# Performance work log

Hardware: AMD Instinct MI355X
Metric: run time of the kernel (lower is better)

Reference implementation:

```python
import jax, jax.numpy as jnp
import numpy as np

B, S, H, NH, DEPTH = 8, 1024, 1024, 16, 24
MLP = int(H * 4.0)
EPS = 1e-6


def _ln(z):
    # flax LayerNorm(use_bias=False, use_scale=False, dtype=bf16): stats in fp32, output bf16
    m = jnp.mean(z, axis=-1, keepdims=True)
    v = jnp.mean(jnp.square(z - m), axis=-1, keepdims=True)
    return ((z - m) * jax.lax.rsqrt(v + EPS)).astype(jnp.bfloat16)


def _modulate(x, shift, scale):
    return x * scale[:, None] + shift[:, None]


def _rms(x):
    return jnp.sqrt(jnp.mean(jnp.square(x)))


def setup_inputs() -> dict:
    key = jax.random.key(0)
    ks = jax.random.split(key, 7)
    init = lambda k, shape, std: (jax.random.normal(k, shape, dtype=jnp.float32) * std)
    return {
        "x": jax.random.normal(ks[0], (B, S, H), dtype=jnp.float32),
        "c": jax.random.normal(ks[1], (B, H), dtype=jnp.float32),
        "w_cond": init(ks[2], (H, 6 * H), 0.02),
        "w_qkv": init(ks[3], (H, 3 * H), 0.02),
        "w_attn_out": init(ks[4], (H, H), 0.02 / np.sqrt(2 * DEPTH)),
        "w_mlp1": init(ks[5], (H, MLP), 0.02),
        "w_mlp2": init(ks[6], (MLP, H), 0.02 / np.sqrt(2 * DEPTH)),
    }


def reference(x, c, w_cond, w_qkv, w_attn_out, w_mlp1, w_mlp2):
    dh = H // NH
    # adaLN conditioning
    cm = jax.nn.silu(c) @ w_cond  # [B, 6H]
    shift_msa, scale_msa, gate_msa, shift_mlp, scale_mlp, gate_mlp = jnp.split(cm, 6, axis=-1)

    # --- attention ---
    x_mod = _modulate(_ln(x), shift_msa, scale_msa)  # fp32 after promote
    kqv = x_mod @ w_qkv
    k, q, v = jnp.split(kqv, 3, axis=-1)
    k = k.reshape(B, S, NH, dh)
    q = q.reshape(B, S, NH, dh) / jnp.sqrt(jnp.float32(dh))
    v = v.reshape(B, S, NH, dh)
    w = jnp.einsum('bqhc,bkhc->bhqk', q, k).astype(jnp.float32)
    w = jax.nn.softmax(w, axis=-1)
    info_max_attn_weight = jnp.mean(jnp.max(w, axis=-1))
    y = jnp.einsum('bhqk,bkhc->bqhc', w, v).reshape(x.shape)
    x_attn = gate_msa[:, None] * (y @ w_attn_out)
    info_attn_norm_ratio = _rms(x_attn) / _rms(x)
    x = x + x_attn

    # --- MLP ---
    x_mod2 = _modulate(_ln(x), shift_mlp, scale_mlp)
    x_mlp = x_mod2 @ w_mlp1
    frac_pos = jnp.mean(x_mlp > 0, axis=(0, 1))
    info_relu_diff = jnp.mean(jnp.abs(frac_pos - 0.5))
    info_relu_zero = jnp.mean(frac_pos == 0)
    info_relu_positive = jnp.mean(frac_pos == 1)
    info_relu_norm = _rms(x_mlp)
    x_mlp = jax.nn.gelu(x_mlp)
    x_mlp = gate_mlp[:, None] * (x_mlp @ w_mlp2)
    info_mlp_norm_ratio = _rms(x_mlp) / _rms(x)
    x = x + x_mlp
    return (x, (info_relu_diff, info_relu_zero, info_relu_positive,
                info_max_attn_weight, info_attn_norm_ratio, info_mlp_norm_ratio,
                info_relu_norm))
```

## Files before the change

### kernel.cpp

```cpp
#include <hip/hip_runtime.h>

typedef unsigned short u16;
typedef __bf16 bf16x8 __attribute__((ext_vector_type(8)));
typedef unsigned short u16x8 __attribute__((ext_vector_type(8)));
typedef float f32x4 __attribute__((ext_vector_type(4)));

union V8 { u16x8 u; bf16x8 b; };

__device__ __forceinline__ u16 f2bf(float f) {
    unsigned u = __float_as_uint(f);
    u += 0x7fffu + ((u >> 16) & 1u);
    return (u16)(u >> 16);
}
__device__ __forceinline__ float bf2f(u16 h) {
    return __uint_as_float(((unsigned)h) << 16);
}

__device__ __forceinline__ void gld16(const void* g, void* l) {
    __builtin_amdgcn_global_load_lds(
        (const __attribute__((address_space(1))) void*)g,
        (__attribute__((address_space(3))) void*)l, 16, 0, 0);
}

__device__ __forceinline__ float block_sum256(float v, float* red) {
#pragma unroll
    for (int mk = 1; mk < 64; mk <<= 1) v += __shfl_xor(v, mk);
    __syncthreads();
    if ((threadIdx.x & 63) == 0) red[threadIdx.x >> 6] = v;
    __syncthreads();
    return red[0] + red[1] + red[2] + red[3];
}

__global__ __launch_bounds__(256)
void cond_kernel(const float* __restrict__ c, const float* __restrict__ w,
                 float* __restrict__ cm) {
    __shared__ float sc[1024];
    const int b = blockIdx.y;
    for (int i = threadIdx.x; i < 1024; i += 256) {
        float v = c[b * 1024 + i];
        sc[i] = v / (1.f + expf(-v));
    }
    __syncthreads();
    const int col = blockIdx.x * 256 + threadIdx.x;
    float acc = 0.f;
    for (int i = 0; i < 1024; ++i) acc += sc[i] * w[(size_t)i * 6144 + col];
    cm[b * 6144 + col] = acc;
}

__global__ __launch_bounds__(256)
void ln_mod_kernel(const float* __restrict__ x, const float* __restrict__ cm,
                   int shift0, int scale0, u16* __restrict__ out) {
    __shared__ float red[8];
    const int row = blockIdx.x, tid = threadIdx.x;
    const int b = row >> 10;
    const float4 v = *(const float4*)(x + (size_t)row * 1024 + tid * 4);
    float s = v.x + v.y + v.z + v.w;
#pragma unroll
    for (int mk = 1; mk < 64; mk <<= 1) s += __shfl_xor(s, mk);
    if ((tid & 63) == 0) red[tid >> 6] = s;
    __syncthreads();
    const float mean = (red[0] + red[1] + red[2] + red[3]) * (1.f / 1024.f);
    const float d0 = v.x - mean, d1 = v.y - mean, d2 = v.z - mean, d3 = v.w - mean;
    float ss = d0 * d0 + d1 * d1 + d2 * d2 + d3 * d3;
#pragma unroll
    for (int mk = 1; mk < 64; mk <<= 1) ss += __shfl_xor(ss, mk);
    if ((tid & 63) == 0) red[4 + (tid >> 6)] = ss;
    __syncthreads();
    const float var = (red[4] + red[5] + red[6] + red[7]) * (1.f / 1024.f);
    const float rs = rsqrtf(var + 1e-6f);
    const float* cmb = cm + b * 6144;
    const int c0 = tid * 4;
    ushort4 ov;
    ov.x = f2bf(bf2f(f2bf(d0 * rs)) * cmb[scale0 + c0 + 0] + cmb[shift0 + c0 + 0]);
    ov.y = f2bf(bf2f(f2bf(d1 * rs)) * cmb[scale0 + c0 + 1] + cmb[shift0 + c0 + 1]);
    ov.z = f2bf(bf2f(f2bf(d2 * rs)) * cmb[scale0 + c0 + 2] + cmb[shift0 + c0 + 2]);
    ov.w = f2bf(bf2f(f2bf(d3 * rs)) * cmb[scale0 + c0 + 3] + cmb[shift0 + c0 + 3]);
    *(ushort4*)(out + (size_t)row * 1024 + c0) = ov;
}

__global__ __launch_bounds__(256)
void transpose_cast(const float* __restrict__ in, u16* __restrict__ out,
                    int R, int C) {
    __shared__ float t[32][33];
    const int tx = threadIdx.x, ty = threadIdx.y;
    const int c0 = blockIdx.x * 32, r0 = blockIdx.y * 32;
#pragma unroll
    for (int i = 0; i < 4; ++i)
        t[ty + i * 8][tx] = in[(size_t)(r0 + ty + i * 8) * C + c0 + tx];
    __syncthreads();
#pragma unroll
    for (int i = 0; i < 4; ++i)
        out[(size_t)(c0 + ty + i * 8) * R + r0 + tx] = f2bf(t[tx][ty + i * 8]);
}

__global__ __launch_bounds__(256)
void vtrans_kernel(const u16* __restrict__ kqv, u16* __restrict__ vT) {
    __shared__ u16 t[32][33];
    const int tx = threadIdx.x, ty = threadIdx.y;
    const int s0 = blockIdx.x * 32, d0 = blockIdx.y * 32;
    const int bh = blockIdx.z, b = bh >> 4, h = bh & 15;
#pragma unroll
    for (int i = 0; i < 4; ++i) {
        int s = s0 + ty + i * 8;
        t[ty + i * 8][tx] = kqv[(size_t)(b * 1024 + s) * 3072 + 2048 + h * 64 + d0 + tx];
    }
    __syncthreads();
#pragma unroll
    for (int i = 0; i < 4; ++i) {
        int d = d0 + ty + i * 8;
        vT[((size_t)bh * 64 + d) * 1024 + s0 + tx] = t[tx][ty + i * 8];
    }
}

template <int EPI>
__global__ __launch_bounds__(256)
void gemm_epi(const u16* __restrict__ A, const u16* __restrict__ BT,
              int M, int N, int K,
              u16* __restrict__ outb, float* __restrict__ outf,
              const float* __restrict__ resid, const float* __restrict__ gatec,
              float* __restrict__ stats, int* __restrict__ counts) {
    __shared__ u16 As[128 * 32];
    __shared__ u16 Bs[128 * 32];
    __shared__ float red[4];
    __shared__ int ccnt[128];

    const int tid = threadIdx.x;
    const int lane = tid & 63;
    const int wave = tid >> 6;
    const int wm = wave & 1, wn = wave >> 1;
    const int quad = lane >> 4, l15 = lane & 15;
    const int tm = blockIdx.y * 128, tn = blockIdx.x * 128;

    const int srow = tid >> 2;
    const int scol = (tid & 3) * 8;

    f32x4 acc[4][4];
#pragma unroll
    for (int i = 0; i < 4; ++i)
#pragma unroll
        for (int j = 0; j < 4; ++j) acc[i][j] = (f32x4){0.f, 0.f, 0.f, 0.f};

    for (int k0 = 0; k0 < K; k0 += 32) {
        __syncthreads();
#pragma unroll
        for (int p = 0; p < 2; ++p) {
            const int r = p * 64 + srow;
            gld16(A + (size_t)(tm + r) * K + k0 + scol, As + p * 2048 + wave * 512);
            gld16(BT + (size_t)(tn + r) * K + k0 + scol, Bs + p * 2048 + wave * 512);
        }
        __syncthreads();
        V8 af[4], bfr[4];
#pragma unroll
        for (int i = 0; i < 4; ++i)
            af[i].u = *(const u16x8*)(As + (wm * 64 + i * 16 + l15) * 32 + quad * 8);
#pragma unroll
        for (int j = 0; j < 4; ++j)
            bfr[j].u = *(const u16x8*)(Bs + (wn * 64 + j * 16 + l15) * 32 + quad * 8);
#pragma unroll
        for (int i = 0; i < 4; ++i)
#pragma unroll
            for (int j = 0; j < 4; ++j)
                acc[i][j] = __builtin_amdgcn_mfma_f32_16x16x32_bf16(
                    af[i].b, bfr[j].b, acc[i][j], 0, 0, 0);
    }

    if (EPI == 2) {
        for (int i = tid; i < 128; i += 256) ccnt[i] = 0;
    }
    __syncthreads();

    float s0 = 0.f, s1 = 0.f, s2 = 0.f;
#pragma unroll
    for (int i = 0; i < 4; ++i) {
#pragma unroll
        for (int j = 0; j < 4; ++j) {
#pragma unroll
            for (int r = 0; r < 4; ++r) {
                const int row = tm + wm * 64 + i * 16 + quad * 4 + r;
                const int col = tn + wn * 64 + j * 16 + l15;
                const float v = acc[i][j][r];
                const size_t idx = (size_t)row * N + col;
                if (EPI == 0) {
                    outb[idx] = f2bf(v);
                } else if (EPI == 1) {
                    const int bb = row >> 10;
                    const float g = gatec[bb * 6144 + col];
                    const float xa = g * v;
                    const float xv = resid[idx];
                    const float o = xv + xa;
                    outf[idx] = o;
                    s0 += xa * xa; s1 += xv * xv; s2 += o * o;
                } else if (EPI == 2) {
                    if (v > 0.f) atomicAdd(&ccnt[wn * 64 + j * 16 + l15], 1);
                    s0 += v * v;
                    const float a = fminf(0.7978845608028654f * (v + 0.044715f * v * v * v), 40.f);
                    const float e = __expf(2.f * a);
                    outb[idx] = f2bf(v * e / (e + 1.f));
                } else {
                    const int bb = row >> 10;
                    const float g = gatec[bb * 6144 + col];
                    const float xm = g * v;
                    const float o = resid[idx] + xm;
                    outf[idx] = o;
                    s0 += xm * xm;
                }
            }
        }
    }

    if (EPI == 1) {
        float t = block_sum256(s0, red); if (tid == 0) atomicAdd(&stats[0], t);
        t = block_sum256(s1, red);       if (tid == 0) atomicAdd(&stats[1], t);
        t = block_sum256(s2, red);       if (tid == 0) atomicAdd(&stats[2], t);
    } else if (EPI == 2) {
        __syncthreads();
        for (int i = tid; i < 128; i += 256) atomicAdd(&counts[tn + i], ccnt[i]);
        float t = block_sum256(s0, red); if (tid == 0) atomicAdd(&stats[3], t);
    } else if (EPI == 3) {
        float t = block_sum256(s0, red); if (tid == 0) atomicAdd(&stats[4], t);
    }
}

__global__ __launch_bounds__(256)
void attn_kernel(const u16* __restrict__ kqv, const u16* __restrict__ vT,
                 u16* __restrict__ y, float* __restrict__ stats) {
    __shared__ u16 Ks[128 * 64];
    __shared__ u16 Vs[64 * 128];
    __shared__ u16 P[4 * 16 * 136];
    const int tid = threadIdx.x, lane = tid & 63, w = tid >> 6;
    const int quad = lane >> 4, l15 = lane & 15;
    const int qt = blockIdx.x, bh = blockIdx.y;
    const int b = bh >> 4, h = bh & 15;
    const int qbase = qt * 64 + w * 16;

    const size_t rowQ = ((size_t)(b * 1024 + qbase + l15)) * 3072 + 1024 + h * 64 + quad * 8;
    V8 aq0, aq1;
    aq0.u = *(const u16x8*)(kqv + rowQ);
    aq1.u = *(const u16x8*)(kqv + rowQ + 32);

    float m[4], l[4];
    f32x4 o[4];
#pragma unroll
    for (int r = 0; r < 4; ++r) { m[r] = -__builtin_inff(); l[r] = 0.f; }
#pragma unroll
    for (int dt = 0; dt < 4; ++dt) o[dt] = (f32x4){0.f, 0.f, 0.f, 0.f};

    u16* wp = P + w * (16 * 136);
    const size_t kbase = (size_t)(b * 1024) * 3072 + h * 64;
    const size_t vbase = (size_t)bh * 65536;

    for (int k0 = 0; k0 < 1024; k0 += 128) {
        __syncthreads();
#pragma unroll
        for (int i = 0; i < 4; ++i) {
            const int c = i * 256 + tid;
            {
                const int row = c >> 3, col8 = (c & 7) ^ (row & 7);
                gld16(kqv + kbase + (size_t)(k0 + row) * 3072 + col8 * 8,
                      Ks + (i * 256 + w * 64) * 8);
            }
            {
                const int d = c >> 4, col8 = (c & 15) ^ (d & 15);
                gld16(vT + vbase + (size_t)d * 1024 + k0 + col8 * 8,
                      Vs + (i * 256 + w * 64) * 8);
            }
        }
        __syncthreads();

        f32x4 sc[8];
#pragma unroll
        for (int jt = 0; jt < 8; ++jt) {
            sc[jt] = (f32x4){0.f, 0.f, 0.f, 0.f};
            const int row = jt * 16 + l15;
            V8 kf0, kf1;
            kf0.u = *(const u16x8*)(Ks + row * 64 + ((quad ^ (l15 & 7)) * 8));
            kf1.u = *(const u16x8*)(Ks + row * 64 + (((quad + 4) ^ (l15 & 7)) * 8));
            sc[jt] = __builtin_amdgcn_mfma_f32_16x16x32_bf16(aq0.b, kf0.b, sc[jt], 0, 0, 0);
            sc[jt] = __builtin_amdgcn_mfma_f32_16x16x32_bf16(aq1.b, kf1.b, sc[jt], 0, 0, 0);
        }

#pragma unroll
        for (int r = 0; r < 4; ++r) {
            float mx = sc[0][r];
#pragma unroll
            for (int jt = 1; jt < 8; ++jt) mx = fmaxf(mx, sc[jt][r]);
            mx *= 0.125f;
#pragma unroll
            for (int mk = 1; mk < 16; mk <<= 1) mx = fmaxf(mx, __shfl_xor(mx, mk));
            const float mn = fmaxf(m[r], mx);
            const float alpha = __expf(m[r] - mn);
            float ps = 0.f;
#pragma unroll
            for (int jt = 0; jt < 8; ++jt) {
                const float p = __expf(sc[jt][r] * 0.125f - mn);
                ps += p;
                wp[(quad * 4 + r) * 136 + jt * 16 + l15] = f2bf(p);
            }
#pragma unroll
            for (int mk = 1; mk < 16; mk <<= 1) ps += __shfl_xor(ps, mk);
            l[r] = l[r] * alpha + ps;
            m[r] = mn;
#pragma unroll
            for (int dt = 0; dt < 4; ++dt) o[dt][r] *= alpha;
        }

#pragma unroll
        for (int j = 0; j < 4; ++j) {
            V8 pa;
            pa.u = *(const u16x8*)(wp + l15 * 136 + j * 32 + quad * 8);
#pragma unroll
            for (int dt = 0; dt < 4; ++dt) {
                const int d = dt * 16 + l15;
                V8 vf;
                vf.u = *(const u16x8*)(Vs + d * 128 + (((j * 4 + quad) ^ l15) * 8));
                o[dt] = __builtin_amdgcn_mfma_f32_16x16x32_bf16(pa.b, vf.b, o[dt], 0, 0, 0);
            }
        }
    }

    float invl[4];
#pragma unroll
    for (int r = 0; r < 4; ++r) invl[r] = 1.f / l[r];
#pragma unroll
    for (int dt = 0; dt < 4; ++dt)
#pragma unroll
        for (int r = 0; r < 4; ++r) {
            const size_t orow = (size_t)(b * 1024 + qbase + quad * 4 + r);
            y[orow * 1024 + h * 64 + dt * 16 + l15] = f2bf(o[dt][r] * invl[r]);
        }

    float sv = (l15 == 0) ? (invl[0] + invl[1] + invl[2] + invl[3]) : 0.f;
#pragma unroll
    for (int mk = 1; mk < 64; mk <<= 1) sv += __shfl_xor(sv, mk);
    if (lane == 0) atomicAdd(&stats[5], sv);
}

__global__ __launch_bounds__(256)
void finalize_kernel(const int* __restrict__ counts, const float* __restrict__ stats,
                     float* __restrict__ out7) {
    __shared__ float red[4];
    float d = 0.f, z = 0.f, pp = 0.f;
    for (int i = threadIdx.x; i < 4096; i += 256) {
        const int c = counts[i];
        const float frac = (float)c * (1.f / 8192.f);
        d += fabsf(frac - 0.5f);
        z += (c == 0) ? 1.f : 0.f;
        pp += (c == 8192) ? 1.f : 0.f;
    }
    d = block_sum256(d, red);
    z = block_sum256(z, red);
    pp = block_sum256(pp, red);
    if (threadIdx.x == 0) {
        out7[0] = d * (1.f / 4096.f);
        out7[1] = z * (1.f / 4096.f);
        out7[2] = pp * (1.f / 4096.f);
        out7[3] = stats[5] * (1.f / 131072.f);
        out7[4] = sqrtf(stats[0] / stats[1]);
        out7[5] = sqrtf(stats[4] / stats[2]);
        out7[6] = sqrtf(stats[3] / (8192.f * 4096.f));
    }
}

extern "C" void kernel_launch(void* const* d_in, const int* in_sizes, int n_in,
                              void* d_out, int out_size, void* d_ws, size_t ws_size,
                              hipStream_t stream) {
    const float* x      = (const float*)d_in[0];
    const float* c      = (const float*)d_in[1];
    const float* w_cond = (const float*)d_in[2];
    const float* w_qkv  = (const float*)d_in[3];
    const float* w_attn = (const float*)d_in[4];
    const float* w_mlp1 = (const float*)d_in[5];
    const float* w_mlp2 = (const float*)d_in[6];
    float* out = (float*)d_out;

    char* base = (char*)d_ws;
    size_t off = 0;
    auto alloc = [&](size_t n) { void* r = base + off; off += (n + 255) & ~(size_t)255; return r; };
    float* stats   = (float*)alloc(64);
    int*   counts  = (int*)alloc(4096 * 4);
    float* cm      = (float*)alloc((size_t)8 * 6144 * 4);
    u16*   x_mod   = (u16*)alloc((size_t)8192 * 1024 * 2);
    u16*   kqv     = (u16*)alloc((size_t)8192 * 3072 * 2);
    u16*   vT      = (u16*)alloc((size_t)128 * 64 * 1024 * 2);
    u16*   y       = (u16*)alloc((size_t)8192 * 1024 * 2);
    float* x1      = (float*)alloc((size_t)8192 * 1024 * 4);
    u16*   wt_qkv  = (u16*)alloc((size_t)3072 * 1024 * 2);
    u16*   wt_attn = (u16*)alloc((size_t)1024 * 1024 * 2);
    u16*   wt_mlp1 = (u16*)alloc((size_t)4096 * 1024 * 2);
    u16*   wt_mlp2 = (u16*)alloc((size_t)1024 * 4096 * 2);
    u16*   h_act   = kqv;
    u16*   x_mod2  = x_mod;
    (void)vT; (void)ws_size; (void)n_in; (void)in_sizes; (void)out_size;

    hipMemsetAsync(d_ws, 0, 256 + 4096 * 4, stream);

    dim3 tb(32, 8);
    transpose_cast<<<dim3(3072 / 32, 1024 / 32), tb, 0, stream>>>(w_qkv,  wt_qkv,  1024, 3072);
    transpose_cast<<<dim3(1024 / 32, 1024 / 32), tb, 0, stream>>>(w_attn, wt_attn, 1024, 1024);
    transpose_cast<<<dim3(4096 / 32, 1024 / 32), tb, 0, stream>>>(w_mlp1, wt_mlp1, 1024, 4096);
    transpose_cast<<<dim3(1024 / 32, 4096 / 32), tb, 0, stream>>>(w_mlp2, wt_mlp2, 4096, 1024);

    cond_kernel<<<dim3(24, 8), 256, 0, stream>>>(c, w_cond, cm);

    ln_mod_kernel<<<8192, 256, 0, stream>>>(x, cm, 0, 1024, x_mod);

    gemm_epi<0><<<dim3(3072 / 128, 8192 / 128), 256, 0, stream>>>(
        x_mod, wt_qkv, 8192, 3072, 1024, kqv, nullptr, nullptr, nullptr, stats, nullptr);

    vtrans_kernel<<<dim3(32, 2, 128), tb, 0, stream>>>(kqv, vT);

    attn_kernel<<<dim3(16, 128), 256, 0, stream>>>(kqv, vT, y, stats);

    gemm_epi<1><<<dim3(1024 / 128, 8192 / 128), 256, 0, stream>>>(
        y, wt_attn, 8192, 1024, 1024, nullptr, x1, x, cm + 2 * 1024, stats, nullptr);

    ln_mod_kernel<<<8192, 256, 0, stream>>>(x1, cm, 3 * 1024, 4 * 1024, x_mod2);

    gemm_epi<2><<<dim3(4096 / 128, 8192 / 128), 256, 0, stream>>>(
        x_mod2, wt_mlp1, 8192, 4096, 1024, h_act, nullptr, nullptr, nullptr, stats, counts);

    gemm_epi<3><<<dim3(1024 / 128, 8192 / 128), 256, 0, stream>>>(
        h_act, wt_mlp2, 8192, 1024, 4096, nullptr, out, x1, cm + 5 * 1024, stats, nullptr);

    finalize_kernel<<<1, 256, 0, stream>>>(counts, stats, out + (size_t)8192 * 1024);
}
```

Measured before the change: 714.4 us.

## Split attention keys across warps with transposed MFMA and cross-warp softmax merge

Reworks the attention kernel so each of the four warps handles all 64 queries of the block but only a 32-key slice of each 128-key tile. It computes transposed scores (K as the A operand, Q as the B operand), so the row reductions need only two cross-lane shuffles. Partial softmax states (m, l, o) are merged across warps through shared memory at the end, and output rows are written as coalesced 16-byte stores. This adds an epilogue reduction, more accumulator registers (64 floats of o per lane), and sets launch bounds to 2 blocks per CU.

```diff
diff --git a/kernel.cpp b/kernel.cpp
--- a/kernel.cpp
+++ b/kernel.cpp
@@ -221,31 +221,42 @@
     }
 }
 
-__global__ __launch_bounds__(256)
+__global__ __launch_bounds__(256, 2)
 void attn_kernel(const u16* __restrict__ kqv, const u16* __restrict__ vT,
                  u16* __restrict__ y, float* __restrict__ stats) {
-    __shared__ u16 Ks[128 * 64];
-    __shared__ u16 Vs[64 * 128];
-    __shared__ u16 P[4 * 16 * 136];
+    __shared__ __align__(16) char smem[49152];
+    u16* Ks = (u16*)smem;
+    u16* Vs = (u16*)(smem + 16384);
+    u16* P  = (u16*)(smem + 32768);
+    float* obuf = (float*)smem;
+    float* mlb  = (float*)(smem + 32768);
+    float* lbuf = (float*)(smem + 32768 + 2048);
+
     const int tid = threadIdx.x, lane = tid & 63, w = tid >> 6;
     const int quad = lane >> 4, l15 = lane & 15;
-    const int qt = blockIdx.x, bh = blockIdx.y;
-    const int b = bh >> 4, h = bh & 15;
-    const int qbase = qt * 64 + w * 16;
-
-    const size_t rowQ = ((size_t)(b * 1024 + qbase + l15)) * 3072 + 1024 + h * 64 + quad * 8;
-    V8 aq0, aq1;
-    aq0.u = *(const u16x8*)(kqv + rowQ);
-    aq1.u = *(const u16x8*)(kqv + rowQ + 32);
+    const int bh = blockIdx.y, b = bh >> 4, h = bh & 15;
+    const int qbase = blockIdx.x * 64;
+    const int fq = (l15 >> 1) & 3;
+
+    V8 qf[4][2];
+#pragma unroll
+    for (int qt = 0; qt < 4; ++qt) {
+        const size_t rq = ((size_t)(b * 1024 + qbase + qt * 16 + l15)) * 3072
+                        + 1024 + h * 64 + quad * 8;
+        qf[qt][0].u = *(const u16x8*)(kqv + rq);
+        qf[qt][1].u = *(const u16x8*)(kqv + rq + 32);
+    }
 
     float m[4], l[4];
-    f32x4 o[4];
-#pragma unroll
-    for (int r = 0; r < 4; ++r) { m[r] = -__builtin_inff(); l[r] = 0.f; }
-#pragma unroll
-    for (int dt = 0; dt < 4; ++dt) o[dt] = (f32x4){0.f, 0.f, 0.f, 0.f};
-
-    u16* wp = P + w * (16 * 136);
+    f32x4 o[4][4];
+#pragma unroll
+    for (int qt = 0; qt < 4; ++qt) { m[qt] = -__builtin_inff(); l[qt] = 0.f; }
+#pragma unroll
+    for (int dt = 0; dt < 4; ++dt)
+#pragma unroll
+        for (int qt = 0; qt < 4; ++qt) o[dt][qt] = (f32x4){0.f, 0.f, 0.f, 0.f};
+
+    u16* wp = P + w * 2048;
     const size_t kbase = (size_t)(b * 1024) * 3072 + h * 64;
     const size_t vbase = (size_t)bh * 65536;
 
@@ -267,72 +278,130 @@
         }
         __syncthreads();
 
-        f32x4 sc[8];
-#pragma unroll
-        for (int jt = 0; jt < 8; ++jt) {
-            sc[jt] = (f32x4){0.f, 0.f, 0.f, 0.f};
-            const int row = jt * 16 + l15;
-            V8 kf0, kf1;
-            kf0.u = *(const u16x8*)(Ks + row * 64 + ((quad ^ (l15 & 7)) * 8));
-            kf1.u = *(const u16x8*)(Ks + row * 64 + (((quad + 4) ^ (l15 & 7)) * 8));
-            sc[jt] = __builtin_amdgcn_mfma_f32_16x16x32_bf16(aq0.b, kf0.b, sc[jt], 0, 0, 0);
-            sc[jt] = __builtin_amdgcn_mfma_f32_16x16x32_bf16(aq1.b, kf1.b, sc[jt], 0, 0, 0);
-        }
-
-#pragma unroll
-        for (int r = 0; r < 4; ++r) {
-            float mx = sc[0][r];
-#pragma unroll
-            for (int jt = 1; jt < 8; ++jt) mx = fmaxf(mx, sc[jt][r]);
+        f32x4 s[2][4];
+#pragma unroll
+        for (int kt = 0; kt < 2; ++kt) {
+            const int krow = w * 32 + kt * 16 + l15;
+            V8 ak0, ak1;
+            ak0.u = *(const u16x8*)(Ks + krow * 64 + ((quad ^ (l15 & 7)) * 8));
+            ak1.u = *(const u16x8*)(Ks + krow * 64 + (((quad + 4) ^ (l15 & 7)) * 8));
+#pragma unroll
+            for (int qt = 0; qt < 4; ++qt) {
+                s[kt][qt] = __builtin_amdgcn_mfma_f32_16x16x32_bf16(
+                    ak0.b, qf[qt][0].b, (f32x4){0.f, 0.f, 0.f, 0.f}, 0, 0, 0);
+                s[kt][qt] = __builtin_amdgcn_mfma_f32_16x16x32_bf16(
+                    ak1.b, qf[qt][1].b, s[kt][qt], 0, 0, 0);
+            }
+        }
+
+#pragma unroll
+        for (int qt = 0; qt < 4; ++qt) {
+            float mx = s[0][qt][0];
+            mx = fmaxf(mx, s[0][qt][1]); mx = fmaxf(mx, s[0][qt][2]);
+            mx = fmaxf(mx, s[0][qt][3]); mx = fmaxf(mx, s[1][qt][0]);
+            mx = fmaxf(mx, s[1][qt][1]); mx = fmaxf(mx, s[1][qt][2]);
+            mx = fmaxf(mx, s[1][qt][3]);
             mx *= 0.125f;
-#pragma unroll
-            for (int mk = 1; mk < 16; mk <<= 1) mx = fmaxf(mx, __shfl_xor(mx, mk));
-            const float mn = fmaxf(m[r], mx);
-            const float alpha = __expf(m[r] - mn);
+            mx = fmaxf(mx, __shfl_xor(mx, 16));
+            mx = fmaxf(mx, __shfl_xor(mx, 32));
+            const float mn = fmaxf(m[qt], mx);
+            const float alpha = __expf(m[qt] - mn);
             float ps = 0.f;
-#pragma unroll
-            for (int jt = 0; jt < 8; ++jt) {
-                const float p = __expf(sc[jt][r] * 0.125f - mn);
-                ps += p;
-                wp[(quad * 4 + r) * 136 + jt * 16 + l15] = f2bf(p);
-            }
-#pragma unroll
-            for (int mk = 1; mk < 16; mk <<= 1) ps += __shfl_xor(ps, mk);
-            l[r] = l[r] * alpha + ps;
-            m[r] = mn;
-#pragma unroll
-            for (int dt = 0; dt < 4; ++dt) o[dt][r] *= alpha;
-        }
-
-#pragma unroll
-        for (int j = 0; j < 4; ++j) {
-            V8 pa;
-            pa.u = *(const u16x8*)(wp + l15 * 136 + j * 32 + quad * 8);
-#pragma unroll
-            for (int dt = 0; dt < 4; ++dt) {
-                const int d = dt * 16 + l15;
-                V8 vf;
-                vf.u = *(const u16x8*)(Vs + d * 128 + (((j * 4 + quad) ^ l15) * 8));
-                o[dt] = __builtin_amdgcn_mfma_f32_16x16x32_bf16(pa.b, vf.b, o[dt], 0, 0, 0);
-            }
-        }
-    }
-
-    float invl[4];
-#pragma unroll
-    for (int r = 0; r < 4; ++r) invl[r] = 1.f / l[r];
-#pragma unroll
-    for (int dt = 0; dt < 4; ++dt)
-#pragma unroll
-        for (int r = 0; r < 4; ++r) {
-            const size_t orow = (size_t)(b * 1024 + qbase + quad * 4 + r);
-            y[orow * 1024 + h * 64 + dt * 16 + l15] = f2bf(o[dt][r] * invl[r]);
-        }
-
-    float sv = (l15 == 0) ? (invl[0] + invl[1] + invl[2] + invl[3]) : 0.f;
-#pragma unroll
-    for (int mk = 1; mk < 64; mk <<= 1) sv += __shfl_xor(sv, mk);
-    if (lane == 0) atomicAdd(&stats[5], sv);
+            u16 pr[2][4];
+#pragma unroll
+            for (int kt = 0; kt < 2; ++kt)
+#pragma unroll
+                for (int r = 0; r < 4; ++r) {
+                    const float p = __expf(s[kt][qt][r] * 0.125f - mn);
+                    ps += p;
+                    pr[kt][r] = f2bf(p);
+                }
+            ps += __shfl_xor(ps, 16);
+            ps += __shfl_xor(ps, 32);
+            l[qt] = l[qt] * alpha + ps;
+            m[qt] = mn;
+#pragma unroll
+            for (int dt = 0; dt < 4; ++dt) o[dt][qt] *= alpha;
+            const int qrow = qt * 16 + l15;
+#pragma unroll
+            for (int kt = 0; kt < 2; ++kt) {
+                const int c0 = (kt * 2 + (quad >> 1)) ^ fq;
+                u16* pdst = wp + qrow * 32 + c0 * 8 + (quad & 1) * 4;
+                *(unsigned*)(pdst)     = (unsigned)pr[kt][0] | ((unsigned)pr[kt][1] << 16);
+                *(unsigned*)(pdst + 2) = (unsigned)pr[kt][2] | ((unsigned)pr[kt][3] << 16);
+            }
+        }
+
+        V8 pb[4];
+#pragma unroll
+        for (int qt = 0; qt < 4; ++qt)
+            pb[qt].u = *(const u16x8*)(wp + (qt * 16 + l15) * 32 + ((quad ^ fq) * 8));
+#pragma unroll
+        for (int dt = 0; dt < 4; ++dt) {
+            V8 av;
+            av.u = *(const u16x8*)(Vs + (dt * 16 + l15) * 128 + (((w * 4 + quad) ^ l15) * 8));
+#pragma unroll
+            for (int qt = 0; qt < 4; ++qt)
+                o[dt][qt] = __builtin_amdgcn_mfma_f32_16x16x32_bf16(
+                    av.b, pb[qt].b, o[dt][qt], 0, 0, 0);
+        }
+    }
+
+    __syncthreads();
+    if (quad == 0) {
+#pragma unroll
+        for (int qt = 0; qt < 4; ++qt) {
+            mlb[(w * 4 + qt) * 16 + l15] = m[qt];
+            mlb[256 + (w * 4 + qt) * 16 + l15] = l[qt];
+        }
+    }
+    __syncthreads();
+    float scale[4];
+#pragma unroll
+    for (int qt = 0; qt < 4; ++qt) {
+        float M = -__builtin_inff();
+#pragma unroll
+        for (int ww = 0; ww < 4; ++ww) M = fmaxf(M, mlb[(ww * 4 + qt) * 16 + l15]);
+        float L = 0.f;
+#pragma unroll
+        for (int ww = 0; ww < 4; ++ww)
+            L += mlb[256 + (ww * 4 + qt) * 16 + l15] *
+                 __expf(mlb[(ww * 4 + qt) * 16 + l15] - M);
+        scale[qt] = __expf(m[qt] - M);
+        if (w == 0 && quad == 0) lbuf[qt * 16 + l15] = 1.f / L;
+    }
+    for (int ww = 0; ww < 4; ++ww) {
+        if (ww == w) {
+#pragma unroll
+            for (int qt = 0; qt < 4; ++qt) {
+                float* dst = obuf + (qt * 16 + l15) * 72 + quad * 4;
+#pragma unroll
+                for (int dt = 0; dt < 4; ++dt) {
+                    f32x4 v = o[dt][qt] * scale[qt];
+                    if (ww != 0) v += *(f32x4*)(dst + dt * 16);
+                    *(f32x4*)(dst + dt * 16) = v;
+                }
+            }
+        }
+        __syncthreads();
+    }
+    if (w == 0) {
+        float sv = lbuf[lane];
+#pragma unroll
+        for (int mk = 1; mk < 64; mk <<= 1) sv += __shfl_xor(sv, mk);
+        if (lane == 0) atomicAdd(&stats[5], sv);
+    }
+    {
+        const int q = tid >> 2, dseg = (tid & 3) * 16;
+        const float il = lbuf[q];
+        const float* src = obuf + q * 72 + dseg;
+        __align__(16) u16 tmp[16];
+#pragma unroll
+        for (int j = 0; j < 16; ++j) tmp[j] = f2bf(src[j] * il);
+        u16* ydst = y + ((size_t)(b * 1024 + qbase + q)) * 1024 + h * 64 + dseg;
+        *(uint4*)(ydst) = *(uint4*)(tmp);
+        *(uint4*)(ydst + 8) = *(uint4*)(tmp + 8);
+    }
 }
 
 __global__ __launch_bounds__(256)
```

Measured after the change: 653.0 us. -8.6%, faster.
